# Optimization experiments

Measured on AMD Instinct MI355X. Metric: run time of the kernel, lower is better.

## Reference

```python
import jax, jax.numpy as jnp
import numpy as np

D = 512      # latent channels (d)
K = 512      # codebook size (k)
PATCH = 8    # encoder conv kernel/stride


def _nearest_embed(z, W):
    """z: (B, D, H, W) latents; W: (D, K) codebook. Returns (quantized (B,D,H,W), argmin (B,H,W))."""
    B, d, H, Wd = z.shape
    zf = z.transpose(0, 2, 3, 1).reshape(-1, d)                      # (N, D)
    # squared L2 distances to each code: ||z||^2 - 2 z.W + ||e||^2
    d2 = (jnp.sum(zf * zf, axis=1, keepdims=True)
          - 2.0 * (zf @ W)
          + jnp.sum(W * W, axis=0))                                   # (N, K)
    idx = jnp.argmin(d2, axis=1)                                      # (N,)
    q = jnp.take(W.T, idx, axis=0)                                    # gather: (N, D)
    q = q.reshape(B, H, Wd, d).transpose(0, 3, 1, 2)
    return q, idx.reshape(B, H, Wd)


def _encode(x, enc_w, enc_b):
    z = jax.lax.conv_general_dilated(x, enc_w, window_strides=(PATCH, PATCH),
                                     padding='VALID',
                                     dimension_numbers=('NCHW', 'OIHW', 'NCHW'))
    return z + enc_b[None, :, None, None]


def _decode(z, dec_w, dec_b):
    y = jax.lax.conv_transpose(z, dec_w, strides=(PATCH, PATCH), padding='VALID',
                               dimension_numbers=('NCHW', 'IOHW', 'NCHW'))
    return y + dec_b[None, :, None, None]


def setup_inputs() -> dict:
    key = jax.random.key(0)
    k1, k2, k3, k4 = jax.random.split(key, 4)
    x = jax.random.normal(k1, (32, 3, 256, 256), dtype=jnp.float32)
    enc_w = jax.random.normal(k2, (D, 3, PATCH, PATCH), dtype=jnp.float32) * 0.02
    enc_b = jnp.zeros((D,), jnp.float32)
    dec_w = jax.random.normal(k3, (D, 3, PATCH, PATCH), dtype=jnp.float32) * 0.02  # IOHW
    dec_b = jnp.zeros((3,), jnp.float32)
    # embedding.weight.normal_(0, 0.02); torch.fmod(weight, 0.04)
    emb_w = jnp.fmod(jax.random.normal(k4, (D, K), dtype=jnp.float32) * 0.02, 0.04)
    return {"x": x, "enc_w": enc_w, "enc_b": enc_b,
            "dec_w": dec_w, "dec_b": dec_b, "emb_w": emb_w}


def reference(x, enc_w, enc_b, dec_w, dec_b, emb_w):
    z_e = _encode(x, enc_w, enc_b)                                    # (32, 512, 32, 32)
    # lookup 1: weight_sg=True (codebook grad stopped) + straight-through estimator
    q1, argmin = _nearest_embed(z_e, jax.lax.stop_gradient(emb_w))
    z_q = z_e + jax.lax.stop_gradient(q1 - z_e)
    # lookup 2: detached encoder output, grads flow to codebook via scatter-add
    emb, _ = _nearest_embed(jax.lax.stop_gradient(z_e), emb_w)
    recon = _decode(z_q, dec_w, dec_b)                                # (32, 3, 256, 256)
    return recon, z_e, emb, argmin
```

## Files before the change

kernel.cpp:

```cpp
#include <hip/hip_runtime.h>
#include <cfloat>

#define PIXB 1024
static const size_t OFF_Z = 6291456;
static const size_t OFF_E = 23068672;
static const size_t OFF_A = 39845888;

typedef __attribute__((address_space(1))) const unsigned int cg_u32;
typedef __attribute__((address_space(3))) unsigned int l_u32;
typedef _Float16 f16x8 __attribute__((ext_vector_type(8)));
typedef _Float16 f16x4 __attribute__((ext_vector_type(4)));
typedef float f32x16 __attribute__((ext_vector_type(16)));

#define SPLIT_SCALE 4096.0f
#define SPLIT_INV   (1.0f / 4096.0f)

#define GL16(srcp, dstp) __builtin_amdgcn_global_load_lds((cg_u32*)(srcp), (l_u32*)(dstp), 16, 0, 0)

__global__ __launch_bounds__(256) void k_prep(const float* __restrict__ W,
                                              const float* __restrict__ dw,
                                              const float* __restrict__ ew,
                                              _Float16* __restrict__ wq,
                                              float* __restrict__ w2,
                                              _Float16* __restrict__ aq,
                                              _Float16* __restrict__ wrow,
                                              _Float16* __restrict__ dwh,
                                              int do_aux) {
  const int t = threadIdx.x;
  const int bx = blockIdx.x;
  __shared__ float T[64][65];
  __shared__ float T2[128][65];
  if (bx < 32) {
    __shared__ float TS[32][260];
    const int cp = bx >> 4, ch = bx & 15;
#pragma unroll
    for (int i = 0; i < 32; ++i)
      TS[i][t] = W[(size_t)(ch * 32 + i) * 512 + cp * 256 + t];
    __syncthreads();
#pragma unroll
    for (int j = 0; j < 4; ++j) {
      const int u = j * 256 + t;
      const int c = u >> 2, kslot = u & 3;
      f16x8 h, l;
#pragma unroll
      for (int jj = 0; jj < 8; ++jj) {
        const float v = TS[kslot * 8 + jj][c];
        const _Float16 hh = (_Float16)v;
        h[jj] = hh;
        l[jj] = (_Float16)((v - (float)hh) * SPLIT_SCALE);
      }
      const int qg = cp * 2 + (c >> 7);
      const int cl = c & 127;
      _Float16* base = wq + qg * 131072 + ch * 8192 + kslot * 1024 + cl * 8;
      *(f16x8*)(base) = h;
      *(f16x8*)(base + 4096) = l;
    }
    return;
  }
  if (bx < 34) {
    const int k = (bx - 32) * 256 + t;
    float acc = 0.f;
    for (int d = 0; d < 512; ++d) { const float v = W[(size_t)d * 512 + k]; acc = fmaf(v, v, acc); }
    w2[k] = acc;
    return;
  }
  if (bx < 46) {
    const int ch = bx - 34;
#pragma unroll
    for (int cc = 0; cc < 2; ++cc) {
      const int c = cc * 256 + t;
      const float* src = ew + (size_t)c * 192 + ch * 16;
#pragma unroll
      for (int slot = 0; slot < 2; ++slot) {
        f16x8 h, l;
#pragma unroll
        for (int j = 0; j < 8; ++j) {
          const float v = src[slot * 8 + j];
          const _Float16 hh = (_Float16)v;
          h[j] = hh;
          l[j] = (_Float16)((v - (float)hh) * SPLIT_SCALE);
        }
        const int se = slot ^ ((c >> 2) & 1);
        _Float16* dst = aq + (size_t)ch * 16384 + c * 16 + se * 8;
        *(f16x8*)dst = h;
        *(f16x8*)(dst + 8192) = l;
      }
    }
    return;
  }
  if (!do_aux) return;
  if (bx < 110) {
    const int id = bx - 46;
    const int c0 = (id & 7) * 64, d0 = (id >> 3) * 64;
#pragma unroll
    for (int i = 0; i < 16; ++i) {
      const int dl = i * 4 + (t >> 6);
      T[dl][t & 63] = W[(size_t)(d0 + dl) * 512 + c0 + (t & 63)];
    }
    __syncthreads();
#pragma unroll
    for (int i = 0; i < 16; ++i) {
      const int cl = i * 4 + (t >> 6);
      const int dl = t & 63;
      wrow[(size_t)(c0 + cl) * 512 + d0 + dl] = (_Float16)T[dl][cl];
    }
    return;
  }
  {
    const int id = bx - 110;
    const int m0 = (id % 3) * 64, d0 = (id / 3) * 128;
#pragma unroll
    for (int i = 0; i < 32; ++i) {
      const int idx = i * 256 + t;
      const int dl = idx >> 6, ml = idx & 63;
      T2[dl][ml] = dw[(size_t)(d0 + dl) * 192 + m0 + ml];
    }
    __syncthreads();
#pragma unroll
    for (int i = 0; i < 32; ++i) {
      const int idx = i * 256 + t;
      const int ml = idx >> 7, dl = idx & 127;
      dwh[(size_t)(m0 + ml) * 512 + d0 + dl] = (_Float16)T2[dl][ml];
    }
  }
}

__global__ __launch_bounds__(512) void k_encmfma(const float* __restrict__ x,
                                                 const _Float16* __restrict__ aq,
                                                 const float* __restrict__ eb,
                                                 float* __restrict__ out) {
  __shared__ __align__(16) unsigned char CB[131072];
  __shared__ float ebL[512];
  const int t = threadIdx.x;
  ebL[t] = eb[t];
  const int w = t >> 6, lane = t & 63;
  const int wc = w & 3, wp = w >> 2;
  const int n0 = blockIdx.x * 64;
  const int b = n0 >> 10, pixbase = n0 & 1023;
  const int i0 = pixbase >> 5;
  const int row = lane & 31, hi = lane >> 5;

  int ab[4];
#pragma unroll
  for (int ct = 0; ct < 4; ++ct) {
    const int c = wc * 128 + ct * 32 + row;
    ab[ct] = c * 32 + ((hi ^ ((c >> 2) & 1)) << 4);
  }
  const int u = t & 255, srow = u >> 6, vsl = u & 63;
  const int csrc = vsl ^ ((vsl >> 3) & 1);
  const float* xb = x + ((size_t)b * 3 * 256 + (i0 + (srow >> 1)) * 8 + (srow & 1)) * 256 + csrc * 4;
  const int bv0 = (((2 * row) ^ ((row >> 2) & 1)) << 4);
  const int bv1 = (((2 * row + 1) ^ ((row >> 2) & 1)) << 4);
  const int brb = wp * 4096 + (wp * 2 + hi) * 1024;

  f32x16 accA[4], accB[4];
#pragma unroll
  for (int ct = 0; ct < 4; ++ct) { accA[ct] = (f32x16)(0.0f); accB[ct] = (f32x16)(0.0f); }

#define STAGE_A(chv) { const _Float16* as_ = aq + (size_t)(chv) * 16384 + t * 8;            \
    char* ad_ = (char*)CB + ((chv) % 3) * 32768 + t * 16;                                   \
    GL16(as_, ad_); GL16(as_ + 4096, ad_ + 8192);                                           \
    GL16(as_ + 8192, ad_ + 16384); GL16(as_ + 12288, ad_ + 24576); }
#define STAGE_B(chv) GL16(xb + (((chv) >> 2) * 65536 + ((chv) & 3) * 512),                  \
                          (char*)CB + 98304 + (((chv) & 3)) * 8192 + t * 16)
#define ECOMP(chv)                                                                          \
  { const char* abuf = (const char*)CB + ((chv) % 3) * 32768;                               \
    const char* bbuf = (const char*)CB + 98304 + ((chv) & 3) * 8192 + brb;                  \
    const float4 xa = *(const float4*)(bbuf + bv0);                                         \
    const float4 xc = *(const float4*)(bbuf + bv1);                                         \
    const float xs[8] = {xa.x, xa.y, xa.z, xa.w, xc.x, xc.y, xc.z, xc.w};                   \
    f16x8 Bh, Bl;                                                                           \
    _Pragma("unroll") for (int q = 0; q < 8; ++q) {                                         \
      const _Float16 hh = (_Float16)xs[q];                                                  \
      Bh[q] = hh; Bl[q] = (_Float16)((xs[q] - (float)hh) * SPLIT_SCALE); }                  \
    __builtin_amdgcn_s_setprio(1);                                                          \
    _Pragma("unroll") for (int ct_ = 0; ct_ < 4; ++ct_) {                                   \
      const f16x8 Ah = *(const f16x8*)(abuf + ab[ct_]);                                     \
      const f16x8 Al = *(const f16x8*)(abuf + 16384 + ab[ct_]);                             \
      accA[ct_] = __builtin_amdgcn_mfma_f32_32x32x16_f16(Ah, Bh, accA[ct_], 0, 0, 0);       \
      accB[ct_] = __builtin_amdgcn_mfma_f32_32x32x16_f16(Ah, Bl, accB[ct_], 0, 0, 0);       \
      accB[ct_] = __builtin_amdgcn_mfma_f32_32x32x16_f16(Al, Bh, accB[ct_], 0, 0, 0); }     \
    __builtin_amdgcn_s_setprio(0); }
#define EPHASE(chv, waitlit)                                                                \
  { asm volatile("s_waitcnt vmcnt(" #waitlit ")" ::: "memory");                             \
    __builtin_amdgcn_sched_barrier(0);                                                      \
    __builtin_amdgcn_s_barrier();                                                           \
    ECOMP(chv);                                                                             \
    __builtin_amdgcn_s_barrier(); }

  STAGE_A(0); STAGE_B(0);
  STAGE_A(1); STAGE_B(1);
  STAGE_B(2);
#pragma unroll 1
  for (int ch = 0; ch < 9; ++ch) {
    STAGE_A(ch + 2);
    STAGE_B(ch + 3);
    EPHASE(ch, 11);
  }
  STAGE_A(11);
  EPHASE(9, 10);
  EPHASE(10, 5);
  EPHASE(11, 0);
#undef STAGE_A
#undef STAGE_B
#undef ECOMP
#undef EPHASE

  const int pl = wp * 32 + row;
#pragma unroll
  for (int ct = 0; ct < 4; ++ct) {
#pragma unroll
    for (int r = 0; r < 16; ++r) {
      const int c = wc * 128 + ct * 32 + (r & 3) + ((r >> 2) << 3) + (hi << 2);
      out[OFF_Z + ((size_t)(b * 512 + c)) * 1024 + pixbase + pl] =
          fmaf(accB[ct][r], SPLIT_INV, accA[ct][r]) + ebL[c];
    }
  }
}

__global__ __launch_bounds__(512) void k_dist(const _Float16* __restrict__ wq,
                                              const float* __restrict__ w2ws,
                                              const float* __restrict__ zin,
                                              float* __restrict__ pv,
                                              int* __restrict__ pi) {
  __shared__ __align__(16) unsigned char CB[73728];
  __shared__ float WV[512];
  __shared__ int   WI[512];
  const int t = threadIdx.x;
  const int w = t >> 6, lane = t & 63;
  const int wc = w & 3, wp = w >> 2;
  const int bid0 = blockIdx.x;
  const int swz = (bid0 & 7) * 256 + (bid0 >> 3);
  const int tile = swz >> 2, q = swz & 3;
  const int n0 = tile * 64;
  const int b = n0 >> 10, pixbase = n0 & 1023;
  const int row = lane & 31, hi = lane >> 5;
  const int pl = wp * 32 + row;

  int abase[2];
#pragma unroll
  for (int ks = 0; ks < 2; ++ks)
    abase[ks] = (2 * ks + hi) * 2048 + (wc * 32 + row) * 16;
  const int swpl = (pl ^ ((pl >> 3) & 3)) * 16;
  const int swln = (lane ^ ((lane >> 3) & 3)) * 16;
  const int twH = (w >> 1) * 1024 + swln + (w & 1) * 8;
  const float* zsrc = zin + OFF_Z + ((size_t)(b * 512 + (t >> 4))) * 1024 + pixbase + (t & 15) * 4;
  const _Float16* wqb = wq + q * 131072;

#define STAGE_W(chv)                                                             \
  { const _Float16* ws_ = wqb + (chv) * 8192 + t * 8;                            \
    char* wd_ = (char*)CB + ((chv) & 1) * 16384 + t * 16;                        \
    GL16(ws_, wd_); GL16(ws_ + 4096, wd_ + 8192); }
#define STAGE_Z(chv)                                                             \
  GL16(zsrc + (size_t)(chv) * 32768,                                             \
       (char*)CB + 32768 + ((chv) % 3) * 8192 + t * 16)
#define TRANSPOSE(chv)                                                           \
  { const char* rb_ = (const char*)CB + 32768 + ((chv) % 3) * 8192;              \
    char* sb_ = (char*)CB + 57344 + ((chv) & 1) * 8192;                          \
    f16x4 hv_, lv_;                                                              \
    _Pragma("unroll") for (int j_ = 0; j_ < 4; ++j_) {                           \
      const float f_ = *(const float*)(rb_ + (4 * w + j_) * 256 + lane * 4);     \
      const _Float16 hh_ = (_Float16)f_;                                         \
      hv_[j_] = hh_;                                                             \
      lv_[j_] = (_Float16)((f_ - (float)hh_) * SPLIT_SCALE); }                   \
    *(f16x4*)(sb_ + twH) = hv_;                                                  \
    *(f16x4*)(sb_ + 4096 + twH) = lv_; }
#define COMPUTE(chv)                                                             \
  { const char* wb_ = (const char*)CB + ((chv) & 1) * 16384;                     \
    const char* zb_ = (const char*)CB + 57344 + ((chv) & 1) * 8192;              \
    const f16x8 Bh0 = *(const f16x8*)(zb_ + hi * 1024 + swpl);                   \
    const f16x8 Bh1 = *(const f16x8*)(zb_ + (2 + hi) * 1024 + swpl);             \
    const f16x8 Bl0 = *(const f16x8*)(zb_ + 4096 + hi * 1024 + swpl);            \
    const f16x8 Bl1 = *(const f16x8*)(zb_ + 4096 + (2 + hi) * 1024 + swpl);      \
    const f16x8 Ah0 = *(const f16x8*)(wb_ + abase[0]);                           \
    const f16x8 Al0 = *(const f16x8*)(wb_ + 8192 + abase[0]);                    \
    const f16x8 Ah1 = *(const f16x8*)(wb_ + abase[1]);                           \
    const f16x8 Al1 = *(const f16x8*)(wb_ + 8192 + abase[1]);                    \
    __builtin_amdgcn_s_setprio(1);                                               \
    accA = __builtin_amdgcn_mfma_f32_32x32x16_f16(Ah0, Bh0, accA, 0, 0, 0);      \
    accB = __builtin_amdgcn_mfma_f32_32x32x16_f16(Ah0, Bl0, accB, 0, 0, 0);      \
    accB = __builtin_amdgcn_mfma_f32_32x32x16_f16(Al0, Bh0, accB, 0, 0, 0);      \
    accA = __builtin_amdgcn_mfma_f32_32x32x16_f16(Ah1, Bh1, accA, 0, 0, 0);      \
    accB = __builtin_amdgcn_mfma_f32_32x32x16_f16(Ah1, Bl1, accB, 0, 0, 0);      \
    accB = __builtin_amdgcn_mfma_f32_32x32x16_f16(Al1, Bh1, accB, 0, 0, 0);      \
    __builtin_amdgcn_s_setprio(0); }
#define LGKM0                                                                    \
  { asm volatile("s_waitcnt lgkmcnt(0)" ::: "memory");                           \
    __builtin_amdgcn_sched_barrier(0); }
#define PHASE_T(chv, waitlit)                                                    \
  { asm volatile("s_waitcnt vmcnt(" #waitlit ")" ::: "memory");                  \
    __builtin_amdgcn_sched_barrier(0);                                           \
    __builtin_amdgcn_s_barrier();                                                \
    TRANSPOSE((chv) + 1);                                                        \
    COMPUTE(chv);                                                                \
    LGKM0;                                                                       \
    __builtin_amdgcn_s_barrier(); }
#define PHASE_F(chv, waitlit)                                                    \
  { asm volatile("s_waitcnt vmcnt(" #waitlit ")" ::: "memory");                  \
    __builtin_amdgcn_sched_barrier(0);                                           \
    __builtin_amdgcn_s_barrier();                                                \
    COMPUTE(chv);                                                                \
    LGKM0;                                                                       \
    __builtin_amdgcn_s_barrier(); }

  f32x16 accA = (f32x16)(0.0f), accB = (f32x16)(0.0f);

  STAGE_W(0);
  STAGE_Z(0); STAGE_Z(1); STAGE_Z(2);
  asm volatile("s_waitcnt vmcnt(2)" ::: "memory");
  __builtin_amdgcn_sched_barrier(0);
  __builtin_amdgcn_s_barrier();
  TRANSPOSE(0);
  LGKM0;
  __builtin_amdgcn_s_barrier();
#pragma unroll 1
  for (int ch = 0; ch < 13; ++ch) {
    STAGE_W(ch + 1);
    STAGE_Z(ch + 3);
    PHASE_T(ch, 4);
  }
  STAGE_W(14);
  PHASE_T(13, 3);
  STAGE_W(15);
  PHASE_T(14, 2);
  PHASE_F(15, 0);

  float bv = FLT_MAX; int bi = 0x7fffffff;
#pragma unroll
  for (int r = 0; r < 16; ++r) {
    const int code = (q << 7) + wc * 32 + ((r & 3) + ((r >> 2) << 3) + (hi << 2));
    const float zw = fmaf(accB[r], SPLIT_INV, accA[r]);
    const float d2 = fmaf(-2.f, zw, w2ws[code]);
    if (d2 < bv || (d2 == bv && code < bi)) { bv = d2; bi = code; }
  }
#undef STAGE_W
#undef STAGE_Z
#undef TRANSPOSE
#undef COMPUTE
#undef LGKM0
#undef PHASE_T
#undef PHASE_F

  WV[w * 64 + lane] = bv;
  WI[w * 64 + lane] = bi;
  __syncthreads();
  if (t < 64) {
    const int pw = t >> 5;
    float fbv = FLT_MAX; int fbi = 0x7fffffff;
#pragma unroll
    for (int wcc = 0; wcc < 4; ++wcc)
#pragma unroll
      for (int hh = 0; hh < 2; ++hh) {
        const int li = (pw * 4 + wcc) * 64 + (t & 31) + hh * 32;
        const float v = WV[li];
        const int ii = WI[li];
        if (v < fbv || (v == fbv && ii < fbi)) { fbv = v; fbi = ii; }
      }
    pv[q * 32768 + n0 + t] = fbv;
    pi[q * 32768 + n0 + t] = fbi;
  }
}

__global__ __launch_bounds__(512) void k_merge(const float* __restrict__ Wc,
                                               const float* __restrict__ pv,
                                               const int* __restrict__ pi,
                                               float* __restrict__ out) {
  __shared__ int IDX[64];
  const int t = threadIdx.x;
  const int n0 = blockIdx.x * 64;
  const int b = n0 >> 10, pixbase = n0 & 1023;
  if (t < 64) {
    float fbv = pv[n0 + t]; int fbi = pi[n0 + t];
#pragma unroll
    for (int q = 1; q < 4; ++q) {
      const float v = pv[q * 32768 + n0 + t];
      const int ii = pi[q * 32768 + n0 + t];
      if (v < fbv || (v == fbv && ii < fbi)) { fbv = v; fbi = ii; }
    }
    out[OFF_A + n0 + t] = (float)fbi;
    IDX[t] = fbi;
  }
  __syncthreads();
  const int pix = t & 63;
  const int kidx = IDX[pix];
  for (int d = t >> 6; d < 512; d += 8)
    out[OFF_E + ((size_t)(b * 512 + d)) * 1024 + pixbase + pix] = Wc[(size_t)d * 512 + kidx];
}

__global__ __launch_bounds__(512) void k_decmfma(const _Float16* __restrict__ wrow,
                                                 const _Float16* __restrict__ dwh,
                                                 const float* __restrict__ db,
                                                 float* __restrict__ out) {
  __shared__ __align__(16) _Float16 QB[2][4096];
  __shared__ int KIDX[128];
  const int t = threadIdx.x;
  const int w = t >> 6, lane = t & 63;
  const int pt = w & 3, mg = w >> 2;
  const int blk = blockIdx.x;
  const int b = blk >> 3;
  const int pixbase = (blk & 7) * 128;
  if (t < 128) KIDX[t] = (int)out[OFF_A + b * 1024 + pixbase + t];
  __syncthreads();
  const int pixS = t >> 2, slotS = t & 3;
  const _Float16* qsrc = wrow + (size_t)KIDX[pixS] * 512 + slotS * 8;
  const int ldsW = pixS * 32 + (slotS ^ ((pixS >> 1) & 3)) * 8;

  const _Float16* abp[3];
#pragma unroll
  for (int mt = 0; mt < 3; ++mt)
    abp[mt] = dwh + (size_t)((mg * 3 + mt) * 32 + (lane & 31)) * 512 + ((lane >> 5) << 3);

  const int brow = pt * 32 + (lane & 31);
  const int bsw = (brow >> 1) & 3;
  int boff[2];
#pragma unroll
  for (int ks = 0; ks < 2; ++ks)
    boff[ks] = brow * 32 + (((ks * 2 + (lane >> 5)) ^ bsw)) * 8;

  f32x16 acc[3];
#pragma unroll
  for (int mt = 0; mt < 3; ++mt) acc[mt] = (f32x16)(0.0f);
  f16x8 A[2][3][2];
  f16x8 qd[2];

  qd[0] = *(const f16x8*)(qsrc);
#pragma unroll
  for (int mt = 0; mt < 3; ++mt)
#pragma unroll
    for (int ks = 0; ks < 2; ++ks)
      A[0][mt][ks] = *(const f16x8*)(abp[mt] + ks * 16);
  *(f16x8*)&QB[0][ldsW] = qd[0];
  qd[1] = *(const f16x8*)(qsrc + 32);
  __syncthreads();

#pragma unroll
  for (int ch = 0; ch < 16; ++ch) {
    const int par = ch & 1;
    if (ch < 15) {
      *(f16x8*)&QB[par ^ 1][ldsW] = qd[(ch + 1) & 1];
#pragma unroll
      for (int mt = 0; mt < 3; ++mt)
#pragma unroll
        for (int ks = 0; ks < 2; ++ks)
          A[par ^ 1][mt][ks] = *(const f16x8*)(abp[mt] + (ch + 1) * 32 + ks * 16);
    }
    if (ch < 14) qd[ch & 1] = *(const f16x8*)(qsrc + (ch + 2) * 32);
    const f16x8 B0 = *(const f16x8*)&QB[par][boff[0]];
    const f16x8 B1 = *(const f16x8*)&QB[par][boff[1]];
#pragma unroll
    for (int mt = 0; mt < 3; ++mt) {
      acc[mt] = __builtin_amdgcn_mfma_f32_32x32x16_f16(A[par][mt][0], B0, acc[mt], 0, 0, 0);
      acc[mt] = __builtin_amdgcn_mfma_f32_32x32x16_f16(A[par][mt][1], B1, acc[mt], 0, 0, 0);
    }
    __syncthreads();
  }

  const float b0 = db[0], b1 = db[1], b2 = db[2];
  const int pix = pixbase + pt * 32 + (lane & 31);
  const int i = pix >> 5, j = pix & 31;
#pragma unroll
  for (int mt = 0; mt < 3; ++mt) {
    const int m0 = (mg * 3 + mt) * 32;
#pragma unroll
    for (int r = 0; r < 16; ++r) {
      const int m = m0 + (r & 3) + ((r >> 2) << 3) + ((lane >> 5) << 2);
      const int c = m >> 6, ki = (m >> 3) & 7, kj = m & 7;
      const float bias = (c == 0) ? b0 : ((c == 1) ? b1 : b2);
      out[(((size_t)b * 3 + c) * 256 + i * 8 + 7 - ki) * 256 + j * 8 + 7 - kj] = acc[mt][r] + bias;
    }
  }
}

__global__ __launch_bounds__(256) void k_decode(const float* __restrict__ dw,
                                                const float* __restrict__ db,
                                                float* out) {
  __shared__ __align__(16) float Qs[32][132];
  __shared__ __align__(16) float Ws3[32][68];
  const int n0 = blockIdx.x * 128;
  const int b = n0 / PIXB, pixbase = n0 % PIXB;
  const int mt = blockIdx.y;
  const int t = threadIdx.x;
  const int pg = t & 31, ck = t >> 5;
  float acc[4][8];
#pragma unroll
  for (int p = 0; p < 4; ++p)
#pragma unroll
    for (int k = 0; k < 8; ++k) acc[p][k] = 0.f;
  for (int dc = 0; dc < 16; ++dc) {
#pragma unroll
    for (int ii = 0; ii < 4; ++ii) {
      const int id = t + ii * 256;
      const int dd = id >> 5, p4 = id & 31;
      *reinterpret_cast<float4*>(&Qs[dd][p4 * 4]) =
        *reinterpret_cast<const float4*>(&out[OFF_E + ((size_t)b * 512 + dc * 32 + dd) * 1024 + pixbase + p4 * 4]);
    }
#pragma unroll
    for (int ii = 0; ii < 2; ++ii) {
      const int id = t + ii * 256;
      const int dd = id >> 4, m4 = id & 15;
      *reinterpret_cast<float4*>(&Ws3[dd][m4 * 4]) =
        *reinterpret_cast<const float4*>(&dw[(size_t)(dc * 32 + dd) * 192 + mt * 64 + m4 * 4]);
    }
    __syncthreads();
#pragma unroll
    for (int dd = 0; dd < 32; ++dd) {
      const float4 qv = *reinterpret_cast<const float4*>(&Qs[dd][pg * 4]);
      const float4 wa = *reinterpret_cast<const float4*>(&Ws3[dd][ck * 8]);
      const float4 wb = *reinterpret_cast<const float4*>(&Ws3[dd][ck * 8 + 4]);
      const float q[4] = {qv.x, qv.y, qv.z, qv.w};
      const float wv[8] = {wa.x, wa.y, wa.z, wa.w, wb.x, wb.y, wb.z, wb.w};
#pragma unroll
      for (int p = 0; p < 4; ++p)
#pragma unroll
        for (int k = 0; k < 8; ++k) acc[p][k] = fmaf(q[p], wv[k], acc[p][k]);
    }
    __syncthreads();
  }
  const int ckg = mt * 8 + ck;
  const int c = ckg >> 3, ki = ckg & 7;
  const float bias = db[c];
#pragma unroll
  for (int p = 0; p < 4; ++p) {
    const int pix = pixbase + pg * 4 + p;
    const int i = pix >> 5, j = pix & 31;
    const size_t base = (((size_t)b * 3 + c) * 256 + i * 8 + 7 - ki) * 256 + j * 8;
#pragma unroll
    for (int kj = 0; kj < 8; ++kj) out[base + 7 - kj] = acc[p][kj] + bias;
  }
}

extern "C" void kernel_launch(void* const* d_in, const int* in_sizes, int n_in,
                              void* d_out, int out_size, void* d_ws, size_t ws_size,
                              hipStream_t stream) {
  const float* x     = (const float*)d_in[0];
  const float* enc_w = (const float*)d_in[1];
  const float* enc_b = (const float*)d_in[2];
  const float* dec_w = (const float*)d_in[3];
  const float* dec_b = (const float*)d_in[4];
  const float* emb_w = (const float*)d_in[5];
  float* out = (float*)d_out;
  float* w2 = (float*)d_ws;
  _Float16* wrow = (_Float16*)((char*)d_ws + 2048);
  _Float16* dwh  = (_Float16*)((char*)d_ws + 2048 + 524288);
  const int do_aux = (ws_size >= (size_t)(2048 + 524288 + 196608)) ? 1 : 0;
  _Float16* wq  = (_Float16*)d_out;
  _Float16* aq  = (_Float16*)((char*)d_out + 2097152);
  float* pv = (float*)((char*)d_out + 4194304);
  int*   pi = (int*)((char*)d_out + 4194304 + 524288);

  k_prep<<<122, 256, 0, stream>>>(emb_w, dec_w, enc_w, wq, w2, aq, wrow, dwh, do_aux);
  k_encmfma<<<512, 512, 0, stream>>>(x, aq, enc_b, out);
  k_dist<<<2048, 512, 0, stream>>>(wq, w2, out, pv, pi);
  k_merge<<<512, 512, 0, stream>>>(emb_w, pv, pi, out);
  if (do_aux)
    k_decmfma<<<256, 512, 0, stream>>>(wrow, dwh, dec_b, out);
  else
    k_decode<<<dim3(256, 3), 256, 0, stream>>>(dec_w, dec_b, out);
}
```

Before: 186.0 us.

## Emit pre-split fp16 hi/lo latents from encoder in MFMA-ready layout for distance kernel

The encoder epilogue now writes, besides the fp32 z_e output, a split hi/lo fp16 copy of the latents into a scratch region of the output buffer. It stages them through LDS with a swizzle so that each pixel's 8-channel groups are contiguous. The distance kernel then loads these fragments directly instead of loading fp32 z, splitting and transposing it in LDS every chunk. This drops the per-chunk transpose phase and shrinks LDS use, at the cost of extra global writes in the encoder and an extra buffer region that must not overlap the real outputs.

```diff
diff --git a/kernel.cpp b/kernel.cpp
--- a/kernel.cpp
+++ b/kernel.cpp
@@ -128,6 +128,7 @@
 __global__ __launch_bounds__(512) void k_encmfma(const float* __restrict__ x,
                                                  const _Float16* __restrict__ aq,
                                                  const float* __restrict__ eb,
+                                                 _Float16* __restrict__ zq2,
                                                  float* __restrict__ out) {
   __shared__ __align__(16) unsigned char CB[131072];
   __shared__ float ebL[512];
@@ -206,24 +207,50 @@
 #undef ECOMP
 #undef EPHASE
 
+  _Float16* ZB = (_Float16*)CB;
   const int pl = wp * 32 + row;
 #pragma unroll
   for (int ct = 0; ct < 4; ++ct) {
+    float zv[16];
 #pragma unroll
     for (int r = 0; r < 16; ++r) {
       const int c = wc * 128 + ct * 32 + (r & 3) + ((r >> 2) << 3) + (hi << 2);
-      out[OFF_Z + ((size_t)(b * 512 + c)) * 1024 + pixbase + pl] =
-          fmaf(accB[ct][r], SPLIT_INV, accA[ct][r]) + ebL[c];
-    }
-  }
+      zv[r] = fmaf(accB[ct][r], SPLIT_INV, accA[ct][r]) + ebL[c];
+      out[OFF_Z + ((size_t)(b * 512 + c)) * 1024 + pixbase + pl] = zv[r];
+    }
+#pragma unroll
+    for (int rq = 0; rq < 4; ++rq) {
+      f16x4 vh, vl;
+#pragma unroll
+      for (int q = 0; q < 4; ++q) {
+        const float f = zv[rq * 4 + q];
+        const _Float16 hh = (_Float16)f;
+        vh[q] = hh;
+        vl[q] = (_Float16)((f - (float)hh) * SPLIT_SCALE);
+      }
+      const int c4 = wc * 128 + ct * 32 + (rq << 3) + (hi << 2);
+      const int off = pl * 1024 + ((c4 * 2) ^ ((pl & 7) << 4));
+      *(f16x4*)((char*)ZB + off) = vh;
+      *(f16x4*)((char*)ZB + 65536 + off) = vl;
+    }
+  }
+  __syncthreads();
+#pragma unroll
+  for (int spl = 0; spl < 2; ++spl)
+#pragma unroll
+    for (int gg = 0; gg < 8; ++gg) {
+      const int g = w * 8 + gg;
+      const f16x8 vv = *(const f16x8*)((char*)ZB + spl * 65536 + lane * 1024 + ((g * 16) ^ ((lane & 7) << 4)));
+      *(f16x8*)(zq2 + ((size_t)(spl * 64 + g) * 32768 + b * 1024 + pixbase + lane) * 8) = vv;
+    }
 }
 
 __global__ __launch_bounds__(512) void k_dist(const _Float16* __restrict__ wq,
                                               const float* __restrict__ w2ws,
-                                              const float* __restrict__ zin,
+                                              const _Float16* __restrict__ zq2,
                                               float* __restrict__ pv,
                                               int* __restrict__ pi) {
-  __shared__ __align__(16) unsigned char CB[73728];
+  __shared__ __align__(16) unsigned char CB[57344];
   __shared__ float WV[512];
   __shared__ int   WI[512];
   const int t = threadIdx.x;
@@ -241,10 +268,8 @@
 #pragma unroll
   for (int ks = 0; ks < 2; ++ks)
     abase[ks] = (2 * ks + hi) * 2048 + (wc * 32 + row) * 16;
-  const int swpl = (pl ^ ((pl >> 3) & 3)) * 16;
-  const int swln = (lane ^ ((lane >> 3) & 3)) * 16;
-  const int twH = (w >> 1) * 1024 + swln + (w & 1) * 8;
-  const float* zsrc = zin + OFF_Z + ((size_t)(b * 512 + (t >> 4))) * 1024 + pixbase + (t & 15) * 4;
+  const _Float16* zsrc = zq2 + ((size_t)((t >> 8) * 64 + ((t >> 6) & 3)) * 32768 +
+                                b * 1024 + pixbase + (t & 63)) * 8;
   const _Float16* wqb = wq + q * 131072;
 
 #define STAGE_W(chv)                                                             \
@@ -252,26 +277,15 @@
     char* wd_ = (char*)CB + ((chv) & 1) * 16384 + t * 16;                        \
     GL16(ws_, wd_); GL16(ws_ + 4096, wd_ + 8192); }
 #define STAGE_Z(chv)                                                             \
-  GL16(zsrc + (size_t)(chv) * 32768,                                             \
+  GL16(zsrc + (size_t)(chv) * 1048576,                                           \
        (char*)CB + 32768 + ((chv) % 3) * 8192 + t * 16)
-#define TRANSPOSE(chv)                                                           \
-  { const char* rb_ = (const char*)CB + 32768 + ((chv) % 3) * 8192;              \
-    char* sb_ = (char*)CB + 57344 + ((chv) & 1) * 8192;                          \
-    f16x4 hv_, lv_;                                                              \
-    _Pragma("unroll") for (int j_ = 0; j_ < 4; ++j_) {                           \
-      const float f_ = *(const float*)(rb_ + (4 * w + j_) * 256 + lane * 4);     \
-      const _Float16 hh_ = (_Float16)f_;                                         \
-      hv_[j_] = hh_;                                                             \
-      lv_[j_] = (_Float16)((f_ - (float)hh_) * SPLIT_SCALE); }                   \
-    *(f16x4*)(sb_ + twH) = hv_;                                                  \
-    *(f16x4*)(sb_ + 4096 + twH) = lv_; }
 #define COMPUTE(chv)                                                             \
   { const char* wb_ = (const char*)CB + ((chv) & 1) * 16384;                     \
-    const char* zb_ = (const char*)CB + 57344 + ((chv) & 1) * 8192;              \
-    const f16x8 Bh0 = *(const f16x8*)(zb_ + hi * 1024 + swpl);                   \
-    const f16x8 Bh1 = *(const f16x8*)(zb_ + (2 + hi) * 1024 + swpl);             \
-    const f16x8 Bl0 = *(const f16x8*)(zb_ + 4096 + hi * 1024 + swpl);            \
-    const f16x8 Bl1 = *(const f16x8*)(zb_ + 4096 + (2 + hi) * 1024 + swpl);      \
+    const char* zb_ = (const char*)CB + 32768 + ((chv) % 3) * 8192;              \
+    const f16x8 Bh0 = *(const f16x8*)(zb_ + hi * 1024 + pl * 16);                \
+    const f16x8 Bh1 = *(const f16x8*)(zb_ + (2 + hi) * 1024 + pl * 16);          \
+    const f16x8 Bl0 = *(const f16x8*)(zb_ + 4096 + hi * 1024 + pl * 16);         \
+    const f16x8 Bl1 = *(const f16x8*)(zb_ + 4096 + (2 + hi) * 1024 + pl * 16);   \
     const f16x8 Ah0 = *(const f16x8*)(wb_ + abase[0]);                           \
     const f16x8 Al0 = *(const f16x8*)(wb_ + 8192 + abase[0]);                    \
     const f16x8 Ah1 = *(const f16x8*)(wb_ + abase[1]);                           \
@@ -287,15 +301,7 @@
 #define LGKM0                                                                    \
   { asm volatile("s_waitcnt lgkmcnt(0)" ::: "memory");                           \
     __builtin_amdgcn_sched_barrier(0); }
-#define PHASE_T(chv, waitlit)                                                    \
-  { asm volatile("s_waitcnt vmcnt(" #waitlit ")" ::: "memory");                  \
-    __builtin_amdgcn_sched_barrier(0);                                           \
-    __builtin_amdgcn_s_barrier();                                                \
-    TRANSPOSE((chv) + 1);                                                        \
-    COMPUTE(chv);                                                                \
-    LGKM0;                                                                       \
-    __builtin_amdgcn_s_barrier(); }
-#define PHASE_F(chv, waitlit)                                                    \
+#define PHASE(chv, waitlit)                                                      \
   { asm volatile("s_waitcnt vmcnt(" #waitlit ")" ::: "memory");                  \
     __builtin_amdgcn_sched_barrier(0);                                           \
     __builtin_amdgcn_s_barrier();                                                \
@@ -306,24 +312,16 @@
   f32x16 accA = (f32x16)(0.0f), accB = (f32x16)(0.0f);
 
   STAGE_W(0);
-  STAGE_Z(0); STAGE_Z(1); STAGE_Z(2);
-  asm volatile("s_waitcnt vmcnt(2)" ::: "memory");
-  __builtin_amdgcn_sched_barrier(0);
-  __builtin_amdgcn_s_barrier();
-  TRANSPOSE(0);
-  LGKM0;
-  __builtin_amdgcn_s_barrier();
+  STAGE_Z(0); STAGE_Z(1);
 #pragma unroll 1
-  for (int ch = 0; ch < 13; ++ch) {
+  for (int ch = 0; ch < 14; ++ch) {
     STAGE_W(ch + 1);
-    STAGE_Z(ch + 3);
-    PHASE_T(ch, 4);
-  }
-  STAGE_W(14);
-  PHASE_T(13, 3);
+    STAGE_Z(ch + 2);
+    PHASE(ch, 4);
+  }
   STAGE_W(15);
-  PHASE_T(14, 2);
-  PHASE_F(15, 0);
+  PHASE(14, 3);
+  PHASE(15, 0);
 
   float bv = FLT_MAX; int bi = 0x7fffffff;
 #pragma unroll
@@ -335,11 +333,9 @@
   }
 #undef STAGE_W
 #undef STAGE_Z
-#undef TRANSPOSE
 #undef COMPUTE
 #undef LGKM0
-#undef PHASE_T
-#undef PHASE_F
+#undef PHASE
 
   WV[w * 64 + lane] = bv;
   WI[w * 64 + lane] = bi;
@@ -547,10 +543,11 @@
   _Float16* aq  = (_Float16*)((char*)d_out + 2097152);
   float* pv = (float*)((char*)d_out + 4194304);
   int*   pi = (int*)((char*)d_out + 4194304 + 524288);
+  _Float16* zq2 = (_Float16*)((char*)d_out + 92274688);
 
   k_prep<<<122, 256, 0, stream>>>(emb_w, dec_w, enc_w, wq, w2, aq, wrow, dwh, do_aux);
-  k_encmfma<<<512, 512, 0, stream>>>(x, aq, enc_b, out);
-  k_dist<<<2048, 512, 0, stream>>>(wq, w2, out, pv, pi);
+  k_encmfma<<<512, 512, 0, stream>>>(x, aq, enc_b, zq2, out);
+  k_dist<<<2048, 512, 0, stream>>>(wq, w2, zq2, pv, pi);
   k_merge<<<512, 512, 0, stream>>>(emb_w, pv, pi, out);
   if (do_aux)
     k_decmfma<<<256, 512, 0, stream>>>(wrow, dwh, dec_b, out);
```

Result: slower. 191.5 us (+2.9%).
